# Kernel optimization log

Measured on AMD Instinct MI355X. Metric: run time of the kernel, lower is better.

Reference implementation:

```python
import jax, jax.numpy as jnp
import numpy as np

MASK_LOGIT_CONST = 1000000000.0
LN_EPS = 1e-12


def setup_inputs() -> dict:
    key = jax.random.key(0)
    k_in, k_w = jax.random.split(key)
    B, S, H = 8, 2048, 1024
    inputs = jax.random.normal(k_in, (B, S, H), dtype=jnp.float32)
    masks = jnp.ones((B, S, S), dtype=jnp.float32)
    w_match = jax.random.normal(k_w, (2 * H, H), dtype=jnp.float32) * (1.0 / np.sqrt(2 * H))
    b_match = jnp.zeros((H,), dtype=jnp.float32)
    ln_gamma = jnp.ones((H,), dtype=jnp.float32)
    ln_beta = jnp.zeros((H,), dtype=jnp.float32)
    return {"inputs": inputs, "masks": masks, "w_match": w_match,
            "b_match": b_match, "ln_gamma": ln_gamma, "ln_beta": ln_beta}


def reference(inputs, masks, w_match, b_match, ln_gamma, ln_beta):
    H = inputs.shape[-1]
    scale = 1.0 / jnp.sqrt(jnp.asarray(H, dtype=inputs.dtype))
    # self-attention scores [B,S,S] (dropout disabled -> query=key=inputs)
    scores = jnp.einsum('bsh,bth->bst', inputs, inputs) * scale
    # logits_mask: scores*mask + (-C)*(1-mask)
    scores = scores * masks - MASK_LOGIT_CONST * (1.0 - masks)
    probs = jax.nn.softmax(scores, axis=-1)
    context = jnp.einsum('bst,bth->bsh', probs, inputs)
    cat = jnp.concatenate([inputs, context], axis=-1)  # [B,S,2H]
    matching = jnp.einsum('bsk,kh->bsh', cat, w_match) + b_match
    # layernorm over last dim
    mu = jnp.mean(matching, axis=-1, keepdims=True)
    var = jnp.mean((matching - mu) ** 2, axis=-1, keepdims=True)
    normed = (matching - mu) * jax.lax.rsqrt(var + LN_EPS)
    return normed * ln_gamma + ln_beta
```

## Files before the change

kernel.cpp:

```cpp
#include <hip/hip_runtime.h>
#include <hip/hip_bf16.h>


typedef unsigned short ushort_t;
typedef __attribute__((ext_vector_type(8))) short short8;
typedef __attribute__((ext_vector_type(4))) float float4v;

__device__ inline float b2f(unsigned int u) {
    union { unsigned int i; float f; } v; v.i = u << 16; return v.f;
}
__device__ inline ushort_t f2b(float f) {
    __hip_bfloat16 h = __float2bfloat16(f);
    return __builtin_bit_cast(ushort_t, h);
}

#define BM 128
#define BN 128
#define BK 64
#define LDSS 72

template<int EPI>
__global__ __launch_bounds__(256, 2)
void gemm_bt(const ushort_t* __restrict__ A, const ushort_t* __restrict__ A2, int kSplit,
             const ushort_t* __restrict__ B,
             int M, int N, int K, int lda, int ldb, int ldc,
             long aBS, long bBS, long cBS,
             const float* __restrict__ mask, long mBS, float scale,
             const float* __restrict__ rowsum,
             const float* __restrict__ bias,
             ushort_t* __restrict__ outb, float* __restrict__ outf)
{
    __shared__ ushort_t As[BM * LDSS];
    __shared__ ushort_t Bs[BN * LDSS];

    const int tid = threadIdx.x;
    const int z = blockIdx.z;
    A  += (size_t)z * aBS;
    A2 += (size_t)z * aBS;
    B  += (size_t)z * bBS;
    if (EPI == 1) mask += (size_t)z * mBS;
    if (EPI == 2) rowsum += (size_t)z * M;
    if (EPI != 3) outb += (size_t)z * cBS;

    const int bm = blockIdx.y * BM;
    const int bn = blockIdx.x * BN;
    const int wave = tid >> 6, lane = tid & 63;
    const int wm = (wave >> 1) * 64, wn = (wave & 1) * 64;
    const int q = lane >> 4, l15 = lane & 15;
    const int sr = tid >> 3;
    const int sc = (tid & 7) * 8;

    float4v acc[4][4];
#pragma unroll
    for (int i = 0; i < 4; i++)
#pragma unroll
        for (int j = 0; j < 4; j++) acc[i][j] = (float4v){0.f, 0.f, 0.f, 0.f};

    for (int k0 = 0; k0 < K; k0 += BK) {
        const ushort_t* aSrc = A;
        int ka = k0;
        if (k0 >= kSplit) { aSrc = A2; ka = k0 - kSplit; }
#pragma unroll
        for (int i = 0; i < 4; i++) {
            const int row = sr + i * 32;
            uint4 av = *(const uint4*)(aSrc + (size_t)(bm + row) * lda + ka + sc);
            uint4 bv = *(const uint4*)(B    + (size_t)(bn + row) * ldb + k0 + sc);
            *(uint4*)(&As[row * LDSS + sc]) = av;
            *(uint4*)(&Bs[row * LDSS + sc]) = bv;
        }
        __syncthreads();
#pragma unroll
        for (int kk = 0; kk < BK; kk += 32) {
            short8 af[4], bfv[4];
#pragma unroll
            for (int mi = 0; mi < 4; mi++)
                af[mi] = *(const short8*)(&As[(wm + mi * 16 + l15) * LDSS + kk + q * 8]);
#pragma unroll
            for (int ni = 0; ni < 4; ni++)
                bfv[ni] = *(const short8*)(&Bs[(wn + ni * 16 + l15) * LDSS + kk + q * 8]);
#pragma unroll
            for (int mi = 0; mi < 4; mi++)
#pragma unroll
                for (int ni = 0; ni < 4; ni++)
                    acc[mi][ni] = __builtin_amdgcn_mfma_f32_16x16x32_bf16(
                        af[mi], bfv[ni], acc[mi][ni], 0, 0, 0);
        }
        __syncthreads();
    }

#pragma unroll
    for (int mi = 0; mi < 4; mi++) {
#pragma unroll
        for (int r = 0; r < 4; r++) {
            const int row = bm + wm + mi * 16 + q * 4 + r;
            const size_t ro = (size_t)row * ldc;
            float rsinv = 1.f;
            if (EPI == 2) rsinv = 1.0f / rowsum[row];
#pragma unroll
            for (int ni = 0; ni < 4; ni++) {
                const int col = bn + wn + ni * 16 + l15;
                float v = acc[mi][ni][r];
                if (EPI == 1) {
                    const float m = mask[(size_t)row * N + col];
                    v = __expf(v * scale * m - 1e9f * (1.0f - m));
                    outb[ro + col] = f2b(v);
                } else if (EPI == 2) {
                    outb[ro + col] = f2b(v * rsinv);
                } else {
                    outf[ro + col] = v + bias[col];
                }
            }
        }
    }
}

__global__ __launch_bounds__(256)
void conv_trans(const float* __restrict__ in, ushort_t* __restrict__ outT,
                ushort_t* __restrict__ outS, int R, int C)
{
    __shared__ float tile[64][65];
    const int tx = threadIdx.x & 15, ty = threadIdx.x >> 4;
    const size_t zoff = (size_t)blockIdx.z * R * C;
    const int r0 = blockIdx.y * 64, c0 = blockIdx.x * 64;
#pragma unroll
    for (int j = 0; j < 4; j++) {
        const int r = ty + j * 16;
        const float4 v = *(const float4*)(in + zoff + (size_t)(r0 + r) * C + c0 + tx * 4);
        tile[r][tx * 4 + 0] = v.x;
        tile[r][tx * 4 + 1] = v.y;
        tile[r][tx * 4 + 2] = v.z;
        tile[r][tx * 4 + 3] = v.w;
        if (outS) {
            ushort4 o;
            o.x = f2b(v.x); o.y = f2b(v.y); o.z = f2b(v.z); o.w = f2b(v.w);
            *(ushort4*)(outS + zoff + (size_t)(r0 + r) * C + c0 + tx * 4) = o;
        }
    }
    __syncthreads();
    ushort_t* tp = outT + zoff;
#pragma unroll
    for (int j = 0; j < 4; j++) {
        const int cc = ty + j * 16;
        ushort4 o;
        o.x = f2b(tile[tx * 4 + 0][cc]);
        o.y = f2b(tile[tx * 4 + 1][cc]);
        o.z = f2b(tile[tx * 4 + 2][cc]);
        o.w = f2b(tile[tx * 4 + 3][cc]);
        *(ushort4*)(tp + (size_t)(c0 + cc) * R + r0 + tx * 4) = o;
    }
}

__global__ __launch_bounds__(256)
void rowsum_k(const ushort_t* __restrict__ E, float* __restrict__ rowsum)
{
    const long row = (long)blockIdx.x * 4 + (threadIdx.x >> 6);
    const int lane = threadIdx.x & 63;
    const ushort_t* p = E + row * 2048;
    float s = 0.f;
#pragma unroll
    for (int i = 0; i < 4; i++) {
        const uint4 u = *(const uint4*)(p + i * 512 + lane * 8);
        s += b2f(u.x & 0xffffu) + b2f(u.x >> 16) + b2f(u.y & 0xffffu) + b2f(u.y >> 16)
           + b2f(u.z & 0xffffu) + b2f(u.z >> 16) + b2f(u.w & 0xffffu) + b2f(u.w >> 16);
    }
#pragma unroll
    for (int off = 32; off > 0; off >>= 1) s += __shfl_down(s, off);
    if (lane == 0) rowsum[row] = s;
}

__global__ __launch_bounds__(256)
void ln_k(const float* __restrict__ Mt, const float* __restrict__ gamma,
          const float* __restrict__ beta, float* __restrict__ out)
{
    const size_t row = blockIdx.x;
    const int tid = threadIdx.x;
    const float4 v = *(const float4*)(Mt + row * 1024 + tid * 4);
    float s  = v.x + v.y + v.z + v.w;
    float s2 = v.x * v.x + v.y * v.y + v.z * v.z + v.w * v.w;
#pragma unroll
    for (int off = 32; off > 0; off >>= 1) {
        s  += __shfl_down(s, off);
        s2 += __shfl_down(s2, off);
    }
    __shared__ float red[8];
    const int wave = tid >> 6, lane = tid & 63;
    if (lane == 0) { red[wave] = s; red[4 + wave] = s2; }
    __syncthreads();
    s  = red[0] + red[1] + red[2] + red[3];
    s2 = red[4] + red[5] + red[6] + red[7];
    const float mu  = s * (1.0f / 1024.0f);
    const float var = s2 * (1.0f / 1024.0f) - mu * mu;
    const float rinv = rsqrtf(var + 1e-12f);
    const float4 g = *(const float4*)(gamma + tid * 4);
    const float4 b = *(const float4*)(beta + tid * 4);
    float4 o;
    o.x = (v.x - mu) * rinv * g.x + b.x;
    o.y = (v.y - mu) * rinv * g.y + b.y;
    o.z = (v.z - mu) * rinv * g.z + b.z;
    o.w = (v.w - mu) * rinv * g.w + b.w;
    *(float4*)(out + row * 1024 + tid * 4) = o;
}

extern "C" void kernel_launch(void* const* d_in, const int* in_sizes, int n_in,
                              void* d_out, int out_size, void* d_ws, size_t ws_size,
                              hipStream_t stream)
{
    const float* X     = (const float*)d_in[0];
    const float* masks = (const float*)d_in[1];
    const float* Wm    = (const float*)d_in[2];
    const float* bias  = (const float*)d_in[3];
    const float* gamma = (const float*)d_in[4];
    const float* beta  = (const float*)d_in[5];
    float* out = (float*)d_out;
    char* ws = (char*)d_ws;

    const int B = 8, S = 2048, H = 1024;

    ushort_t* Xb  = (ushort_t*)(ws);
    ushort_t* XT  = (ushort_t*)(ws + 33554432);
    ushort_t* WT  = (ushort_t*)(ws + 67108864);
    ushort_t* E   = (ushort_t*)(ws + 71303168);
    float*    rs  = (float*)   (ws + 138412032);
    ushort_t* CTX = (ushort_t*)(ws + 138477568);
    float* matching = (float*)E;

    conv_trans<<<dim3(16, 32, 8), 256, 0, stream>>>(X, XT, Xb, S, H);
    conv_trans<<<dim3(16, 32, 1), 256, 0, stream>>>(Wm, WT, nullptr, 2 * H, H);

    const float scale = 0.03125f;

    gemm_bt<1><<<dim3(16, 16, 8), 256, 0, stream>>>(
        Xb, Xb, 1 << 30, Xb,
        S, S, H, H, H, S,
        (long)S * H, (long)S * H, (long)S * S,
        masks, (long)S * S, scale, nullptr, nullptr, E, nullptr);

    rowsum_k<<<(B * S) / 4, 256, 0, stream>>>(E, rs);

    gemm_bt<2><<<dim3(8, 16, 8), 256, 0, stream>>>(
        E, E, 1 << 30, XT,
        S, H, S, S, S, H,
        (long)S * S, (long)H * S, (long)S * H,
        nullptr, 0, 1.0f, rs, nullptr, CTX, nullptr);

    gemm_bt<3><<<dim3(8, 128, 1), 256, 0, stream>>>(
        Xb, CTX, H, WT,
        B * S, H, 2 * H, H, 2 * H, H,
        0, 0, 0,
        nullptr, 0, 1.0f, nullptr, bias, nullptr, matching);

    ln_k<<<B * S, 256, 0, stream>>>(matching, gamma, beta, out);
}
```

Before: 550.8 us.

## Use direct global-to-LDS loads with XOR swizzle and fuse softmax rowsum into GEMM

The GEMM tile loads now go straight from global memory into LDS through global_load_lds, replacing the register round-trip. The padded LDS layout is replaced by an XOR-swizzled unpadded layout to avoid bank conflicts. The separate rowsum kernel is removed: the exp epilogue of the scores GEMM reduces each row within the wave and atomically adds it into a zeroed rowsum buffer. This saves a full pass over the large exp matrix, at the cost of atomics and a memset.

Result: no change. 552.8 us (+0.4%).

```diff
diff --git a/kernel.cpp b/kernel.cpp
--- a/kernel.cpp
+++ b/kernel.cpp
@@ -14,10 +14,15 @@
     return __builtin_bit_cast(ushort_t, h);
 }
 
+__device__ inline void gload_lds16(const ushort_t* g, ushort_t* lds) {
+    __builtin_amdgcn_global_load_lds(
+        (const __attribute__((address_space(1))) unsigned int*)g,
+        (__attribute__((address_space(3))) unsigned int*)lds, 16, 0, 0);
+}
+
 #define BM 128
 #define BN 128
 #define BK 64
-#define LDSS 72
 
 template<int EPI>
 __global__ __launch_bounds__(256, 2)
@@ -26,12 +31,12 @@
              int M, int N, int K, int lda, int ldb, int ldc,
              long aBS, long bBS, long cBS,
              const float* __restrict__ mask, long mBS, float scale,
-             const float* __restrict__ rowsum,
+             float* __restrict__ rowsum,
              const float* __restrict__ bias,
              ushort_t* __restrict__ outb, float* __restrict__ outf)
 {
-    __shared__ ushort_t As[BM * LDSS];
-    __shared__ ushort_t Bs[BN * LDSS];
+    __shared__ __align__(16) ushort_t As[BM * BK];
+    __shared__ __align__(16) ushort_t Bs[BN * BK];
 
     const int tid = threadIdx.x;
     const int z = blockIdx.z;
@@ -39,7 +44,7 @@
     A2 += (size_t)z * aBS;
     B  += (size_t)z * bBS;
     if (EPI == 1) mask += (size_t)z * mBS;
-    if (EPI == 2) rowsum += (size_t)z * M;
+    if (EPI == 1 || EPI == 2) rowsum += (size_t)z * M;
     if (EPI != 3) outb += (size_t)z * cBS;
 
     const int bm = blockIdx.y * BM;
@@ -47,8 +52,8 @@
     const int wave = tid >> 6, lane = tid & 63;
     const int wm = (wave >> 1) * 64, wn = (wave & 1) * 64;
     const int q = lane >> 4, l15 = lane & 15;
-    const int sr = tid >> 3;
-    const int sc = (tid & 7) * 8;
+    const int lrow = lane >> 3;
+    const int cswz = (lane & 7) ^ lrow;
 
     float4v acc[4][4];
 #pragma unroll
@@ -61,23 +66,28 @@
         int ka = k0;
         if (k0 >= kSplit) { aSrc = A2; ka = k0 - kSplit; }
 #pragma unroll
-        for (int i = 0; i < 4; i++) {
-            const int row = sr + i * 32;
-            uint4 av = *(const uint4*)(aSrc + (size_t)(bm + row) * lda + ka + sc);
-            uint4 bv = *(const uint4*)(B    + (size_t)(bn + row) * ldb + k0 + sc);
-            *(uint4*)(&As[row * LDSS + sc]) = av;
-            *(uint4*)(&Bs[row * LDSS + sc]) = bv;
+        for (int j = 0; j < 4; j++) {
+            const int p = wave * 4 + j;
+            const int ro = p * 8 + lrow;
+            gload_lds16(aSrc + (size_t)(bm + ro) * lda + ka + cswz * 8, &As[p * 512]);
+            gload_lds16(B    + (size_t)(bn + ro) * ldb + k0 + cswz * 8, &Bs[p * 512]);
         }
         __syncthreads();
 #pragma unroll
         for (int kk = 0; kk < BK; kk += 32) {
             short8 af[4], bfv[4];
 #pragma unroll
-            for (int mi = 0; mi < 4; mi++)
-                af[mi] = *(const short8*)(&As[(wm + mi * 16 + l15) * LDSS + kk + q * 8]);
-#pragma unroll
-            for (int ni = 0; ni < 4; ni++)
-                bfv[ni] = *(const short8*)(&Bs[(wn + ni * 16 + l15) * LDSS + kk + q * 8]);
+            for (int mi = 0; mi < 4; mi++) {
+                const int lr = wm + mi * 16 + l15;
+                const int kc = (kk >> 3) + q;
+                af[mi] = *(const short8*)(&As[lr * 64 + ((kc ^ (lr & 7)) << 3)]);
+            }
+#pragma unroll
+            for (int ni = 0; ni < 4; ni++) {
+                const int lr = wn + ni * 16 + l15;
+                const int kc = (kk >> 3) + q;
+                bfv[ni] = *(const short8*)(&Bs[lr * 64 + ((kc ^ (lr & 7)) << 3)]);
+            }
 #pragma unroll
             for (int mi = 0; mi < 4; mi++)
 #pragma unroll
@@ -96,6 +106,7 @@
             const size_t ro = (size_t)row * ldc;
             float rsinv = 1.f;
             if (EPI == 2) rsinv = 1.0f / rowsum[row];
+            float s = 0.f;
 #pragma unroll
             for (int ni = 0; ni < 4; ni++) {
                 const int col = bn + wn + ni * 16 + l15;
@@ -103,12 +114,20 @@
                 if (EPI == 1) {
                     const float m = mask[(size_t)row * N + col];
                     v = __expf(v * scale * m - 1e9f * (1.0f - m));
+                    s += v;
                     outb[ro + col] = f2b(v);
                 } else if (EPI == 2) {
                     outb[ro + col] = f2b(v * rsinv);
                 } else {
                     outf[ro + col] = v + bias[col];
                 }
+            }
+            if (EPI == 1) {
+                s += __shfl_xor(s, 8);
+                s += __shfl_xor(s, 4);
+                s += __shfl_xor(s, 2);
+                s += __shfl_xor(s, 1);
+                if (l15 == 0) atomicAdd(&rowsum[row], s);
             }
         }
     }
@@ -148,24 +167,6 @@
         o.w = f2b(tile[tx * 4 + 3][cc]);
         *(ushort4*)(tp + (size_t)(c0 + cc) * R + r0 + tx * 4) = o;
     }
-}
-
-__global__ __launch_bounds__(256)
-void rowsum_k(const ushort_t* __restrict__ E, float* __restrict__ rowsum)
-{
-    const long row = (long)blockIdx.x * 4 + (threadIdx.x >> 6);
-    const int lane = threadIdx.x & 63;
-    const ushort_t* p = E + row * 2048;
-    float s = 0.f;
-#pragma unroll
-    for (int i = 0; i < 4; i++) {
-        const uint4 u = *(const uint4*)(p + i * 512 + lane * 8);
-        s += b2f(u.x & 0xffffu) + b2f(u.x >> 16) + b2f(u.y & 0xffffu) + b2f(u.y >> 16)
-           + b2f(u.z & 0xffffu) + b2f(u.z >> 16) + b2f(u.w & 0xffffu) + b2f(u.w >> 16);
-    }
-#pragma unroll
-    for (int off = 32; off > 0; off >>= 1) s += __shfl_down(s, off);
-    if (lane == 0) rowsum[row] = s;
 }
 
 __global__ __launch_bounds__(256)
@@ -226,6 +227,7 @@
 
     conv_trans<<<dim3(16, 32, 8), 256, 0, stream>>>(X, XT, Xb, S, H);
     conv_trans<<<dim3(16, 32, 1), 256, 0, stream>>>(Wm, WT, nullptr, 2 * H, H);
+    hipMemsetAsync(rs, 0, (size_t)B * S * sizeof(float), stream);
 
     const float scale = 0.03125f;
 
@@ -233,9 +235,7 @@
         Xb, Xb, 1 << 30, Xb,
         S, S, H, H, H, S,
         (long)S * H, (long)S * H, (long)S * S,
-        masks, (long)S * S, scale, nullptr, nullptr, E, nullptr);
-
-    rowsum_k<<<(B * S) / 4, 256, 0, stream>>>(E, rs);
+        masks, (long)S * S, scale, rs, nullptr, E, nullptr);
 
     gemm_bt<2><<<dim3(8, 16, 8), 256, 0, stream>>>(
         E, E, 1 << 30, XT,
```
